# Kernel tuning notes

Measured on AMD Instinct MI355X. Metric: run time of the kernel, lower is better.

## Reference

```python
import jax, jax.numpy as jnp
import numpy as np
from jax import lax
from jax.scipy.special import logsumexp

B, S, H = 64, 512, 768
NUM_TAG, NUM_POS = 17, 45


def setup_inputs() -> dict:
    key = jax.random.key(0)
    ks = jax.random.split(key, 12)
    return {
        "hidden": jax.random.normal(ks[0], (B, S, H), dtype=jnp.float32),
        "mask": jnp.ones((B, S), dtype=jnp.int32),
        "target_tag": jax.random.randint(ks[1], (B, S), 0, NUM_TAG).astype(jnp.int64),
        "target_pos": jax.random.randint(ks[2], (B, S), 0, NUM_POS).astype(jnp.int64),
        "W_tag": jax.random.normal(ks[3], (H, NUM_TAG), dtype=jnp.float32) * 0.02,
        "b_tag": jnp.zeros((NUM_TAG,), dtype=jnp.float32),
        "W_pos": jax.random.normal(ks[4], (H, NUM_POS), dtype=jnp.float32) * 0.02,
        "b_pos": jnp.zeros((NUM_POS,), dtype=jnp.float32),
        "start_tag": jax.random.normal(ks[5], (NUM_TAG,), dtype=jnp.float32) * 0.1,
        "trans_tag": jax.random.normal(ks[6], (NUM_TAG, NUM_TAG), dtype=jnp.float32) * 0.1,
        "end_tag": jax.random.normal(ks[7], (NUM_TAG,), dtype=jnp.float32) * 0.1,
        "start_pos": jax.random.normal(ks[8], (NUM_POS,), dtype=jnp.float32) * 0.1,
        "trans_pos": jax.random.normal(ks[9], (NUM_POS, NUM_POS), dtype=jnp.float32) * 0.1,
        "end_pos": jax.random.normal(ks[10], (NUM_POS,), dtype=jnp.float32) * 0.1,
    }


def crf_nll(emissions, tags, mask, start, trans, end):
    """torchcrf negative log-likelihood, reduction='mean'. emissions:[B,S,T]."""
    e = jnp.swapaxes(emissions, 0, 1)            # [S,B,T]
    tg = jnp.swapaxes(tags, 0, 1)                # [S,B]
    m = jnp.swapaxes(mask, 0, 1).astype(emissions.dtype)  # [S,B]
    # --- numerator: score of the target path ---
    first = start[tg[0]] + jnp.take_along_axis(e[0], tg[0][:, None], 1)[:, 0]

    def num_step(carry, x):
        prev_tag, score = carry
        et, tt, mt = x
        s = trans[prev_tag, tt] + jnp.take_along_axis(et, tt[:, None], 1)[:, 0]
        score = score + s * mt
        prev_tag = jnp.where(mt > 0, tt, prev_tag)
        return (prev_tag, score), None

    (last_tag, num), _ = lax.scan(num_step, (tg[0], first), (e[1:], tg[1:], m[1:]))
    num = num + end[last_tag]
    # --- denominator: forward algorithm (log-sum-exp scan) ---
    score0 = start[None, :] + e[0]               # [B,T]

    def den_step(score, x):
        et, mt = x
        nxt = logsumexp(score[:, :, None] + trans[None, :, :] + et[:, None, :], axis=1)
        return jnp.where(mt[:, None] > 0, nxt, score), None

    den, _ = lax.scan(den_step, score0, (e[1:], m[1:]))
    den = logsumexp(den + end[None, :], axis=1)
    return -jnp.mean(num - den)


def crf_decode(emissions, mask, start, trans, end):
    """Viterbi decode; returns best tag paths [B,S] (int32)."""
    T = emissions.shape[-1]
    e = jnp.swapaxes(emissions, 0, 1)            # [S,B,T]
    m = jnp.swapaxes(mask, 0, 1)                 # [S,B]
    score0 = start[None, :] + e[0]

    def fwd_step(score, x):
        et, mt = x
        cand = score[:, :, None] + trans[None, :, :]     # [B,T,T]
        idx = jnp.argmax(cand, axis=1).astype(jnp.int32)  # [B,T] best prev tag
        nxt = jnp.max(cand, axis=1) + et
        keep = (mt > 0)[:, None]
        score = jnp.where(keep, nxt, score)
        idx = jnp.where(keep, idx, jnp.arange(T, dtype=jnp.int32)[None, :])
        return score, idx

    score, hist = lax.scan(fwd_step, score0, (e[1:], m[1:]))  # hist:[S-1,B,T]
    score = score + end[None, :]
    last = jnp.argmax(score, axis=1).astype(jnp.int32)        # [B]

    def back_step(tag, idx):
        prev = jnp.take_along_axis(idx, tag[:, None], 1)[:, 0]
        return prev, tag

    tag0, path = lax.scan(back_step, last, hist, reverse=True)  # path:[S-1,B]
    full = jnp.concatenate([tag0[None, :], path], axis=0)       # [S,B]
    return jnp.swapaxes(full, 0, 1)


def reference(hidden, mask, target_tag, target_pos,
              W_tag, b_tag, W_pos, b_pos,
              start_tag, trans_tag, end_tag,
              start_pos, trans_pos, end_pos):
    # dropout is identity in eval mode
    tag = jnp.einsum('bsh,ht->bst', hidden, W_tag) + b_tag   # [B,S,T]
    pos = jnp.einsum('bsh,hp->bsp', hidden, W_pos) + b_pos   # [B,S,P]
    loss_tag = crf_nll(jax.nn.log_softmax(tag, axis=2), target_tag, mask,
                       start_tag, trans_tag, end_tag)
    loss_pos = crf_nll(jax.nn.log_softmax(pos, axis=2), target_pos, mask,
                       start_pos, trans_pos, end_pos)
    pred_tag = crf_decode(tag, mask, start_tag, trans_tag, end_tag)
    pred_pos = crf_decode(pos, mask, start_pos, trans_pos, end_pos)
    return pred_tag, pred_pos, loss_tag, loss_pos
```

## Files before the change

### kernel.cpp

```cpp
#include <hip/hip_runtime.h>
#include <cmath>
#include <cstdint>
#include <cstddef>

#define NT 17
#define NP 45
#define CH 8

__device__ __forceinline__ float rlane(float v, int k) {
    return __int_as_float(__builtin_amdgcn_readlane(__float_as_int(v), k));
}

__global__ __launch_bounds__(256) void gemm_logits(
    const float* __restrict__ hidden, const float* __restrict__ Wt,
    const float* __restrict__ bt, const float* __restrict__ Wp,
    const float* __restrict__ bp, float* __restrict__ tagL,
    float* __restrict__ posL)
{
    __shared__ float As[32 * 68];
    __shared__ float Bs[32 * 64];
    const int tid = threadIdx.x;
    const int rg = tid >> 4;
    const int cg = tid & 15;
    const int row0 = blockIdx.x * 64;

    float acc[4][4];
#pragma unroll
    for (int a = 0; a < 4; ++a)
#pragma unroll
        for (int b = 0; b < 4; ++b) acc[a][b] = 0.f;

    for (int kc = 0; kc < 768; kc += 32) {
        __syncthreads();
#pragma unroll
        for (int it = 0; it < 2; ++it) {
            int idx = tid + it * 256;
            int r = idx >> 3, q = idx & 7;
            float4 h = *(const float4*)(hidden + (size_t)(row0 + r) * 768 + kc + q * 4);
            As[(q * 4 + 0) * 68 + r] = h.x;
            As[(q * 4 + 1) * 68 + r] = h.y;
            As[(q * 4 + 2) * 68 + r] = h.z;
            As[(q * 4 + 3) * 68 + r] = h.w;
        }
#pragma unroll
        for (int it = 0; it < 8; ++it) {
            int idx = tid + it * 256;
            int k = idx >> 6, c = idx & 63;
            float v = 0.f;
            if (c < NT) v = Wt[(kc + k) * NT + c];
            else if (c < NT + NP) v = Wp[(kc + k) * NP + (c - NT)];
            Bs[idx] = v;
        }
        __syncthreads();
#pragma unroll
        for (int kk = 0; kk < 32; ++kk) {
            float4 a4 = *(const float4*)(As + kk * 68 + rg * 4);
            float4 b4 = *(const float4*)(Bs + kk * 64 + cg * 4);
            float av[4] = {a4.x, a4.y, a4.z, a4.w};
            float bv[4] = {b4.x, b4.y, b4.z, b4.w};
#pragma unroll
            for (int jr = 0; jr < 4; ++jr)
#pragma unroll
                for (int jc = 0; jc < 4; ++jc)
                    acc[jr][jc] = fmaf(av[jr], bv[jc], acc[jr][jc]);
        }
    }
#pragma unroll
    for (int jr = 0; jr < 4; ++jr) {
        size_t r = (size_t)row0 + rg * 4 + jr;
#pragma unroll
        for (int jc = 0; jc < 4; ++jc) {
            int c = cg * 4 + jc;
            if (c < NT) tagL[r * NT + c] = acc[jr][jc] + bt[c];
            else if (c < NT + NP) posL[r * NP + (c - NT)] = acc[jr][jc] + bp[c - NT];
        }
    }
}

template <int T, int PAD>
__device__ void nll_scan(int b,
    const float* __restrict__ logits, const int* __restrict__ mask,
    const int* __restrict__ targ, const float* __restrict__ start,
    const float* __restrict__ trans, const float* __restrict__ endv,
    float* __restrict__ den, float* __restrict__ num)
{
    const int lane = threadIdx.x;
    const int jj = (lane < T) ? lane : (T - 1);
    float Ecol[PAD];
#pragma unroll
    for (int i = 0; i < PAD; ++i) Ecol[i] = (i < T) ? __expf(trans[i * T + jj]) : 0.f;
    const float esjj = __expf(start[jj]);
    const float* eptr = logits + (size_t)b * 512 * T + jj;
    const int* mptr = mask + b * 512;

    float eb[CH], en[CH], fb[CH];
    int mb, mn = 0;
#pragma unroll
    for (int k = 0; k < CH; ++k) { eb[k] = eptr[k * T]; en[k] = 0.f; }
    mb = mptr[lane & (CH - 1)];

    float a = 0.f;
    int excorr = 0;
    for (int c = 0; c < 64; ++c) {
        unsigned long long kb = __ballot(mb > 0);
        if (c < 63) {
            const float* ep2 = eptr + (c + 1) * CH * T;
#pragma unroll
            for (int k = 0; k < CH; ++k) en[k] = ep2[k * T];
            mn = mptr[(c + 1) * CH + (lane & (CH - 1))];
        }
#pragma unroll
        for (int k = 0; k < CH; ++k) fb[k] = __expf(eb[k]);
#pragma unroll
        for (int s = 0; s < CH; ++s) {
            float d0 = 0.f, d1 = 0.f, d2 = 0.f, d3 = 0.f;
#pragma unroll
            for (int q = 0; q < PAD / 4; ++q) {
                d0 = fmaf(rlane(a, 4 * q + 0), Ecol[4 * q + 0], d0);
                d1 = fmaf(rlane(a, 4 * q + 1), Ecol[4 * q + 1], d1);
                d2 = fmaf(rlane(a, 4 * q + 2), Ecol[4 * q + 2], d2);
                d3 = fmaf(rlane(a, 4 * q + 3), Ecol[4 * q + 3], d3);
            }
            float cand = ((d0 + d1) + (d2 + d3)) * fb[s];
            bool keep = (kb >> s) & 1ULL;
            bool first = (c == 0) && (s == 0);
            a = first ? (esjj * fb[0]) : (keep ? cand : a);
        }
        float m = a;
#pragma unroll
        for (int o = 32; o; o >>= 1) m = fmaxf(m, __shfl_xor(m, o));
        int ex;
        (void)frexpf(m, &ex);
        a *= ldexpf(1.0f, -ex);
        excorr += ex;
#pragma unroll
        for (int k = 0; k < CH; ++k) eb[k] = en[k];
        mb = mn;
    }
    float term = (lane < T) ? a * __expf(endv[lane]) : 0.f;
#pragma unroll
    for (int o = 32; o; o >>= 1) term += __shfl_xor(term, o);
    if (lane == 0) den[b] = __logf(term) + (float)excorr * 0.69314718056f;

    float part = 0.f; int Lc = 0;
    for (int t = lane; t < 512; t += 64) {
        int mt = mask[b * 512 + t];
        Lc += (mt > 0);
        if (t >= 1 && mt > 0) {
            int tg = targ[b * 512 + t];
            int pg = targ[b * 512 + t - 1];
            part += trans[pg * T + tg] + logits[((size_t)b * 512 + t) * T + tg];
        }
    }
#pragma unroll
    for (int o = 32; o; o >>= 1) { part += __shfl_xor(part, o); Lc += __shfl_xor(Lc, o); }
    if (lane == 0) {
        int t0g = targ[b * 512];
        num[b] = start[t0g] + logits[(size_t)b * 512 * T + t0g]
               + part + endv[targ[b * 512 + Lc - 1]];
    }
}

template <int T, int PAD>
__device__ void vit_fwd(int b,
    const float* __restrict__ logits, const int* __restrict__ mask,
    const float* __restrict__ start, const float* __restrict__ trans,
    float* __restrict__ score)
{
    const int lane = threadIdx.x;
    const int jj = (lane < T) ? lane : (T - 1);
    float Tcol[PAD];
#pragma unroll
    for (int i = 0; i < PAD; ++i) Tcol[i] = (i < T) ? trans[i * T + jj] : -1e30f;
    const float sjj = start[jj];
    const float* eptr = logits + (size_t)b * 512 * T + jj;
    const int* mptr = mask + b * 512;
    float* sptr = score + (size_t)b * 512 * T + lane;

    float eb[CH], en[CH];
    int mb, mn = 0;
#pragma unroll
    for (int k = 0; k < CH; ++k) { eb[k] = eptr[k * T]; en[k] = 0.f; }
    mb = mptr[lane & (CH - 1)];

    float sc = 0.f;
    for (int c = 0; c < 64; ++c) {
        unsigned long long kb = __ballot(mb > 0);
        if (c < 63) {
            const float* ep2 = eptr + (c + 1) * CH * T;
#pragma unroll
            for (int k = 0; k < CH; ++k) en[k] = ep2[k * T];
            mn = mptr[(c + 1) * CH + (lane & (CH - 1))];
        }
#pragma unroll
        for (int s = 0; s < CH; ++s) {
            float m = -1e30f;
#pragma unroll
            for (int q = 0; q < PAD / 4; ++q) {
                float ca = rlane(sc, 4 * q + 0) + Tcol[4 * q + 0];
                float cb = rlane(sc, 4 * q + 1) + Tcol[4 * q + 1];
                float cc = rlane(sc, 4 * q + 2) + Tcol[4 * q + 2];
                float cd = rlane(sc, 4 * q + 3) + Tcol[4 * q + 3];
                m = fmaxf(m, fmaxf(ca, cb));
                m = fmaxf(m, fmaxf(cc, cd));
            }
            float nxt = m + eb[s];
            bool keep = (kb >> s) & 1ULL;
            bool first = (c == 0) && (s == 0);
            sc = first ? (sjj + eb[0]) : (keep ? nxt : sc);
            if (lane < T) sptr[(size_t)(c * CH + s) * T] = sc;
        }
#pragma unroll
        for (int k = 0; k < CH; ++k) eb[k] = en[k];
        mb = mn;
    }
}

__global__ __launch_bounds__(64, 1) void scan_kernel(
    const float* tagL, const float* posL, const int* mask,
    const int* tgT, const int* tgP,
    const float* startT, const float* transT, const float* endT,
    const float* startP, const float* transP, const float* endP,
    float* scoreT, float* scoreP,
    float* denT, float* denP, float* numT, float* numP)
{
    int bid = blockIdx.x;
    if (bid < 64)
        vit_fwd<NP, 48>(bid, posL, mask, startP, transP, scoreP);
    else if (bid < 128)
        nll_scan<NP, 48>(bid - 64, posL, mask, tgP, startP, transP, endP, denP, numP);
    else if (bid < 192)
        vit_fwd<NT, 20>(bid - 128, tagL, mask, startT, transT, scoreT);
    else
        nll_scan<NT, 20>(bid - 192, tagL, mask, tgT, startT, transT, endT, denT, numT);
}

template <int T>
__device__ void hist_block(int b, int tc,
    const float* __restrict__ score, const int* __restrict__ mask,
    const float* __restrict__ trans, unsigned char* __restrict__ hist)
{
    const int wave = threadIdx.x >> 6;
    const int lane = threadIdx.x & 63;
    const int jj = (lane < T) ? lane : (T - 1);
    float Tcol[T];
#pragma unroll
    for (int i = 0; i < T; ++i) Tcol[i] = trans[i * T + jj];
    for (int q = 0; q < 16; ++q) {
        int t = tc * 64 + wave * 16 + q;
        if (t < 1) continue;
        int mt = mask[b * 512 + t];
        int hv;
        if (mt > 0) {
            float sv = score[((size_t)b * 512 + t - 1) * T + jj];
            float mx = -1e30f; int am = 0;
#pragma unroll
            for (int i = 0; i < T; ++i) {
                float cand = rlane(sv, i) + Tcol[i];
                bool g = cand > mx;
                mx = g ? cand : mx;
                am = g ? i : am;
            }
            hv = am;
        } else {
            hv = jj;
        }
        if (lane < T)
            hist[((size_t)b * 512 + (t - 1)) * T + lane] = (unsigned char)hv;
    }
}

__global__ __launch_bounds__(256) void hist_kernel(
    const float* scoreT, const float* scoreP, const int* mask,
    const float* transT, const float* transP,
    unsigned char* histT, unsigned char* histP)
{
    int blk = blockIdx.x;
    if (blk < 512) hist_block<NP>(blk >> 3, blk & 7, scoreP, mask, transP, histP);
    else { blk -= 512; hist_block<NT>(blk >> 3, blk & 7, scoreT, mask, transT, histT); }
}

template <int T>
__device__ void backtrace(int b, const float* __restrict__ score,
    const unsigned char* __restrict__ hist, const float* __restrict__ endv,
    float* __restrict__ outp, unsigned char* sh)
{
    unsigned char* h  = sh;
    unsigned char* g2 = sh + 512 * T;
    unsigned char* g4 = sh + 1024 * T;
    unsigned char* g8 = sh + 1024 * T + 128 * T;
    unsigned char* pr = sh + 1024 * T + 192 * T;
    const int lane = threadIdx.x;

    {
        const int4* src = (const int4*)(hist + (size_t)b * 512 * T);
        int4* dst = (int4*)h;
        int n16 = (512 * T) / 16;
        for (int i = lane; i < n16; i += 64) dst[i] = src[i];
    }
    __syncthreads();
    for (int idx = lane; idx < 510 * T; idx += 64) {
        int r = idx / T, i = idx - r * T;
        g2[idx] = h[r * T + h[(r + 1) * T + i]];
    }
    __syncthreads();
    for (int idx = lane; idx < 127 * T; idx += 64) {
        int a4 = idx / T, i = idx - a4 * T;
        int r = 3 + 4 * a4;
        g4[idx] = g2[r * T + g2[(r + 2) * T + i]];
    }
    __syncthreads();
    for (int idx = lane; idx < 63 * T; idx += 64) {
        int a = idx / T, i = idx - a * T;
        int r = 503 - 8 * a;
        int a4lo = (r - 3) >> 2, a4hi = (r + 1) >> 2;
        g8[idx] = g4[a4lo * T + g4[a4hi * T + i]];
    }
    float v = (lane < T) ? (score[((size_t)b * 512 + 511) * T + lane] + endv[lane]) : -1e30f;
    float mx = v;
#pragma unroll
    for (int o = 32; o; o >>= 1) mx = fmaxf(mx, __shfl_xor(mx, o));
    unsigned long long bal = __ballot(v == mx);
    int cur = __ffsll(bal) - 1;
    __syncthreads();
    int myCur = 0;
    for (int a = 0; a < 64; ++a) {
        if (lane == a) myCur = cur;
        if (a < 63) cur = g8[a * T + cur];
    }
    {
        int ta = 511 - 8 * lane;
        int j = myCur;
        pr[ta] = (unsigned char)j;
        int rlo = (lane == 63) ? 0 : (ta - 7);
        for (int r = ta - 1; r >= rlo; --r) {
            j = h[r * T + j];
            pr[r] = (unsigned char)j;
        }
    }
    __syncthreads();
    for (int k = lane; k < 512; k += 64)
        outp[(size_t)b * 512 + k] = (float)pr[k];
}

__global__ __launch_bounds__(64, 1) void backtrace_kernel(
    const float* scoreT, const float* scoreP,
    const unsigned char* histT, const unsigned char* histP,
    const float* endT, const float* endP, float* out)
{
    __shared__ __align__(16) unsigned char sh[1216 * NP + 576];
    int blk = blockIdx.x;
    if (blk < 64) backtrace<NP>(blk, scoreP, histP, endP, out + 32768, sh);
    else backtrace<NT>(blk - 64, scoreT, histT, endT, out, sh);
}

__global__ __launch_bounds__(64) void finalize_kernel(
    const float* numT, const float* denT, const float* numP, const float* denP,
    float* out)
{
    int lane = threadIdx.x;
    float dT = numT[lane] - denT[lane];
    float dP = numP[lane] - denP[lane];
#pragma unroll
    for (int o = 32; o; o >>= 1) { dT += __shfl_xor(dT, o); dP += __shfl_xor(dP, o); }
    if (lane == 0) {
        out[65536] = -dT / 64.f;
        out[65537] = -dP / 64.f;
    }
}

extern "C" void kernel_launch(void* const* d_in, const int* in_sizes, int n_in,
                              void* d_out, int out_size, void* d_ws, size_t ws_size,
                              hipStream_t stream)
{
    const float* hidden = (const float*)d_in[0];
    const int*   mask   = (const int*)d_in[1];
    const int*   tgT    = (const int*)d_in[2];
    const int*   tgP    = (const int*)d_in[3];
    const float* Wt     = (const float*)d_in[4];
    const float* bt     = (const float*)d_in[5];
    const float* Wp     = (const float*)d_in[6];
    const float* bp     = (const float*)d_in[7];
    const float* startT = (const float*)d_in[8];
    const float* transT = (const float*)d_in[9];
    const float* endT   = (const float*)d_in[10];
    const float* startP = (const float*)d_in[11];
    const float* transP = (const float*)d_in[12];
    const float* endP   = (const float*)d_in[13];

    float* ws     = (float*)d_ws;
    float* tagL   = ws;
    float* posL   = tagL + 557056;
    float* scoreT = posL + 1474560;
    float* scoreP = scoreT + 557056;
    float* denT   = scoreP + 1474560;
    float* denP   = denT + 64;
    float* numT   = denP + 64;
    float* numP   = numT + 64;
    unsigned char* histT = (unsigned char*)(numP + 64);
    unsigned char* histP = histT + (size_t)64 * 512 * NT;
    float* out = (float*)d_out;

    gemm_logits<<<512, 256, 0, stream>>>(hidden, Wt, bt, Wp, bp, tagL, posL);
    scan_kernel<<<256, 64, 0, stream>>>(tagL, posL, mask, tgT, tgP,
        startT, transT, endT, startP, transP, endP,
        scoreT, scoreP, denT, denP, numT, numP);
    hist_kernel<<<1024, 256, 0, stream>>>(scoreT, scoreP, mask, transT, transP,
        histT, histP);
    backtrace_kernel<<<128, 64, 0, stream>>>(scoreT, scoreP, histT, histP,
        endT, endP, out);
    finalize_kernel<<<1, 64, 0, stream>>>(numT, denT, numP, denP, out);
}
```

Measured before the change: 498.9 us.

## Rewrite logits GEMM as LDS-free wave-per-8-rows kernel with broadcast hidden loads

Replaces the shared-memory tiled GEMM with a design where each lane owns one output column (62 total) and each wave computes 8 rows. Hidden rows are read as uniform 8-float vector loads, the same for every lane, and weights are prefetched one k-chunk ahead in registers. The grid doubles to 1024 blocks of 32 rows each. The aim is to drop the LDS staging and the barriers on a memory-bound skinny GEMM, at the cost of strided uncoalesced weight loads and two idle lanes per wave.

```diff
diff --git a/kernel.cpp b/kernel.cpp
--- a/kernel.cpp
+++ b/kernel.cpp
@@ -6,6 +6,8 @@
 #define NT 17
 #define NP 45
 #define CH 8
+
+typedef float f32x8 __attribute__((ext_vector_type(8)));
 
 __device__ __forceinline__ float rlane(float v, int k) {
     return __int_as_float(__builtin_amdgcn_readlane(__float_as_int(v), k));
@@ -17,62 +19,57 @@
     const float* __restrict__ bp, float* __restrict__ tagL,
     float* __restrict__ posL)
 {
-    __shared__ float As[32 * 68];
-    __shared__ float Bs[32 * 64];
-    const int tid = threadIdx.x;
-    const int rg = tid >> 4;
-    const int cg = tid & 15;
-    const int row0 = blockIdx.x * 64;
-
-    float acc[4][4];
-#pragma unroll
-    for (int a = 0; a < 4; ++a)
-#pragma unroll
-        for (int b = 0; b < 4; ++b) acc[a][b] = 0.f;
-
-    for (int kc = 0; kc < 768; kc += 32) {
-        __syncthreads();
-#pragma unroll
-        for (int it = 0; it < 2; ++it) {
-            int idx = tid + it * 256;
-            int r = idx >> 3, q = idx & 7;
-            float4 h = *(const float4*)(hidden + (size_t)(row0 + r) * 768 + kc + q * 4);
-            As[(q * 4 + 0) * 68 + r] = h.x;
-            As[(q * 4 + 1) * 68 + r] = h.y;
-            As[(q * 4 + 2) * 68 + r] = h.z;
-            As[(q * 4 + 3) * 68 + r] = h.w;
-        }
-#pragma unroll
-        for (int it = 0; it < 8; ++it) {
-            int idx = tid + it * 256;
-            int k = idx >> 6, c = idx & 63;
-            float v = 0.f;
-            if (c < NT) v = Wt[(kc + k) * NT + c];
-            else if (c < NT + NP) v = Wp[(kc + k) * NP + (c - NT)];
-            Bs[idx] = v;
-        }
-        __syncthreads();
-#pragma unroll
-        for (int kk = 0; kk < 32; ++kk) {
-            float4 a4 = *(const float4*)(As + kk * 68 + rg * 4);
-            float4 b4 = *(const float4*)(Bs + kk * 64 + cg * 4);
-            float av[4] = {a4.x, a4.y, a4.z, a4.w};
-            float bv[4] = {b4.x, b4.y, b4.z, b4.w};
-#pragma unroll
-            for (int jr = 0; jr < 4; ++jr)
-#pragma unroll
-                for (int jc = 0; jc < 4; ++jc)
-                    acc[jr][jc] = fmaf(av[jr], bv[jc], acc[jr][jc]);
-        }
-    }
-#pragma unroll
-    for (int jr = 0; jr < 4; ++jr) {
-        size_t r = (size_t)row0 + rg * 4 + jr;
-#pragma unroll
-        for (int jc = 0; jc < 4; ++jc) {
-            int c = cg * 4 + jc;
-            if (c < NT) tagL[r * NT + c] = acc[jr][jc] + bt[c];
-            else if (c < NT + NP) posL[r * NP + (c - NT)] = acc[jr][jc] + bp[c - NT];
+    const int lane = threadIdx.x & 63;
+    const int wid  = __builtin_amdgcn_readfirstlane(threadIdx.x >> 6);
+    const int c = (lane < 62) ? lane : 61;
+    const bool isTag = (c < NT);
+    const float* wbase = isTag ? (Wt + c) : (Wp + (c - NT));
+    const int wstride = isTag ? NT : NP;
+    const float bias = isTag ? bt[c] : bp[c - NT];
+
+    const int row0 = blockIdx.x * 32 + wid * 8;
+    const float* h0 = hidden + (size_t)row0 * 768;
+
+    float acc[8];
+#pragma unroll
+    for (int r = 0; r < 8; ++r) acc[r] = 0.f;
+
+    float wv[8], wn[8];
+#pragma unroll
+    for (int j = 0; j < 8; ++j) wv[j] = wbase[(size_t)j * wstride];
+
+    for (int kc = 0; kc < 768; kc += 8) {
+        if (kc + 8 < 768) {
+#pragma unroll
+            for (int j = 0; j < 8; ++j)
+                wn[j] = wbase[(size_t)(kc + 8 + j) * wstride];
+        }
+        f32x8 hv[8];
+#pragma unroll
+        for (int r = 0; r < 8; ++r)
+            hv[r] = *(const f32x8*)(h0 + (size_t)r * 768 + kc);
+#pragma unroll
+        for (int r = 0; r < 8; ++r) {
+            acc[r] = fmaf(hv[r][0], wv[0], acc[r]);
+            acc[r] = fmaf(hv[r][1], wv[1], acc[r]);
+            acc[r] = fmaf(hv[r][2], wv[2], acc[r]);
+            acc[r] = fmaf(hv[r][3], wv[3], acc[r]);
+            acc[r] = fmaf(hv[r][4], wv[4], acc[r]);
+            acc[r] = fmaf(hv[r][5], wv[5], acc[r]);
+            acc[r] = fmaf(hv[r][6], wv[6], acc[r]);
+            acc[r] = fmaf(hv[r][7], wv[7], acc[r]);
+        }
+#pragma unroll
+        for (int j = 0; j < 8; ++j) wv[j] = wn[j];
+    }
+
+    if (lane < 62) {
+#pragma unroll
+        for (int r = 0; r < 8; ++r) {
+            float v = acc[r] + bias;
+            size_t row = (size_t)row0 + r;
+            if (isTag) tagL[row * NT + c] = v;
+            else       posL[row * NP + (c - NT)] = v;
         }
     }
 }
@@ -401,7 +398,7 @@
     unsigned char* histP = histT + (size_t)64 * 512 * NT;
     float* out = (float*)d_out;
 
-    gemm_logits<<<512, 256, 0, stream>>>(hidden, Wt, bt, Wp, bp, tagL, posL);
+    gemm_logits<<<1024, 256, 0, stream>>>(hidden, Wt, bt, Wp, bp, tagL, posL);
     scan_kernel<<<256, 64, 0, stream>>>(tagL, posL, mask, tgT, tgP,
         startT, transT, endT, startP, transP, endP,
         scoreT, scoreP, denT, denP, numT, numP);
```

Measured after the change: 538.8 us. 1.08x slower.

## Use direct global-to-LDS loads with swizzled A tile and prepacked weights in GEMM

Applied to the files above, without the earlier changes.

Adds a pre-pass that packs the tag and POS weight matrices into one zero-padded 768x64 buffer, so the GEMM can load B tiles with plain 16-byte loads. Both A and B tiles now go straight from global memory into LDS through the async global_load_lds builtin, and the A tile is stored row-major with an XOR swizzle instead of being transposed through registers. The inner loop is restructured into 4-wide k chunks. Separately, the scan's per-chunk max reduction now reads only the first T lanes with readlane instead of doing a full 64-lane shuffle. The packed weights live in the scoreT workspace region, which scan_kernel overwrites later, and this adds one extra kernel launch.

```diff
diff --git a/kernel.cpp b/kernel.cpp
--- a/kernel.cpp
+++ b/kernel.cpp
@@ -11,17 +11,36 @@
     return __int_as_float(__builtin_amdgcn_readlane(__float_as_int(v), k));
 }
 
+__device__ __forceinline__ void gload16(const float* g, float* l) {
+    __builtin_amdgcn_global_load_lds(
+        (const __attribute__((address_space(1))) void*)g,
+        (__attribute__((address_space(3))) void*)l, 16, 0, 0);
+}
+
+__global__ __launch_bounds__(256) void pack_w(
+    const float* __restrict__ Wt, const float* __restrict__ Wp,
+    float* __restrict__ Wpk)
+{
+    int i = blockIdx.x * 256 + threadIdx.x;
+    if (i >= 768 * 64) return;
+    int k = i >> 6, c = i & 63;
+    float v = 0.f;
+    if (c < NT) v = Wt[k * NT + c];
+    else if (c < NT + NP) v = Wp[k * NP + (c - NT)];
+    Wpk[i] = v;
+}
+
 __global__ __launch_bounds__(256) void gemm_logits(
-    const float* __restrict__ hidden, const float* __restrict__ Wt,
-    const float* __restrict__ bt, const float* __restrict__ Wp,
-    const float* __restrict__ bp, float* __restrict__ tagL,
-    float* __restrict__ posL)
-{
-    __shared__ float As[32 * 68];
-    __shared__ float Bs[32 * 64];
+    const float* __restrict__ hidden, const float* __restrict__ Wpk,
+    const float* __restrict__ bt, const float* __restrict__ bp,
+    float* __restrict__ tagL, float* __restrict__ posL)
+{
+    __shared__ __align__(16) float As[64 * 32];
+    __shared__ __align__(16) float Bs[32 * 64];
     const int tid = threadIdx.x;
     const int rg = tid >> 4;
     const int cg = tid & 15;
+    const int srg = rg & 7;
     const int row0 = blockIdx.x * 64;
 
     float acc[4][4];
@@ -30,40 +49,51 @@
 #pragma unroll
         for (int b = 0; b < 4; ++b) acc[a][b] = 0.f;
 
+    const int arow = tid >> 3;
+    const int aq   = tid & 7;
+    const int bk   = tid >> 4;
+    const int bc4  = tid & 15;
+
+#pragma unroll 1
     for (int kc = 0; kc < 768; kc += 32) {
+        {
+            int r0 = arow;
+            int s0 = (r0 >> 2) & 7;
+            gload16(hidden + (size_t)(row0 + r0) * 768 + kc + ((aq ^ s0) << 2),
+                    As + r0 * 32 + aq * 4);
+            int r1 = 32 + arow;
+            int s1 = (r1 >> 2) & 7;
+            gload16(hidden + (size_t)(row0 + r1) * 768 + kc + ((aq ^ s1) << 2),
+                    As + r1 * 32 + aq * 4);
+            gload16(Wpk + (size_t)(kc + bk) * 64 + bc4 * 4,
+                    Bs + bk * 64 + bc4 * 4);
+            gload16(Wpk + (size_t)(kc + 16 + bk) * 64 + bc4 * 4,
+                    Bs + (16 + bk) * 64 + bc4 * 4);
+        }
         __syncthreads();
 #pragma unroll
-        for (int it = 0; it < 2; ++it) {
-            int idx = tid + it * 256;
-            int r = idx >> 3, q = idx & 7;
-            float4 h = *(const float4*)(hidden + (size_t)(row0 + r) * 768 + kc + q * 4);
-            As[(q * 4 + 0) * 68 + r] = h.x;
-            As[(q * 4 + 1) * 68 + r] = h.y;
-            As[(q * 4 + 2) * 68 + r] = h.z;
-            As[(q * 4 + 3) * 68 + r] = h.w;
-        }
-#pragma unroll
-        for (int it = 0; it < 8; ++it) {
-            int idx = tid + it * 256;
-            int k = idx >> 6, c = idx & 63;
-            float v = 0.f;
-            if (c < NT) v = Wt[(kc + k) * NT + c];
-            else if (c < NT + NP) v = Wp[(kc + k) * NP + (c - NT)];
-            Bs[idx] = v;
+        for (int k4 = 0; k4 < 8; ++k4) {
+            const int qb = ((k4 ^ srg) << 2);
+            float a_[4][4], b_[4][4];
+#pragma unroll
+            for (int jr = 0; jr < 4; ++jr) {
+                float4 t = *(const float4*)(As + (rg * 4 + jr) * 32 + qb);
+                a_[jr][0] = t.x; a_[jr][1] = t.y; a_[jr][2] = t.z; a_[jr][3] = t.w;
+            }
+#pragma unroll
+            for (int kk = 0; kk < 4; ++kk) {
+                float4 t = *(const float4*)(Bs + (k4 * 4 + kk) * 64 + cg * 4);
+                b_[kk][0] = t.x; b_[kk][1] = t.y; b_[kk][2] = t.z; b_[kk][3] = t.w;
+            }
+#pragma unroll
+            for (int kk = 0; kk < 4; ++kk)
+#pragma unroll
+                for (int jr = 0; jr < 4; ++jr)
+#pragma unroll
+                    for (int jc = 0; jc < 4; ++jc)
+                        acc[jr][jc] = fmaf(a_[jr][kk], b_[kk][jc], acc[jr][jc]);
         }
         __syncthreads();
-#pragma unroll
-        for (int kk = 0; kk < 32; ++kk) {
-            float4 a4 = *(const float4*)(As + kk * 68 + rg * 4);
-            float4 b4 = *(const float4*)(Bs + kk * 64 + cg * 4);
-            float av[4] = {a4.x, a4.y, a4.z, a4.w};
-            float bv[4] = {b4.x, b4.y, b4.z, b4.w};
-#pragma unroll
-            for (int jr = 0; jr < 4; ++jr)
-#pragma unroll
-                for (int jc = 0; jc < 4; ++jc)
-                    acc[jr][jc] = fmaf(av[jr], bv[jc], acc[jr][jc]);
-        }
     }
 #pragma unroll
     for (int jr = 0; jr < 4; ++jr) {
@@ -126,9 +156,16 @@
             bool first = (c == 0) && (s == 0);
             a = first ? (esjj * fb[0]) : (keep ? cand : a);
         }
-        float m = a;
-#pragma unroll
-        for (int o = 32; o; o >>= 1) m = fmaxf(m, __shfl_xor(m, o));
+        float mv0 = rlane(a, 0), mv1 = rlane(a, 1);
+        float mv2 = rlane(a, 2), mv3 = rlane(a, 3);
+#pragma unroll
+        for (int i = 4; i < T; i += 4) {
+            mv0 = fmaxf(mv0, rlane(a, i + 0));
+            mv1 = fmaxf(mv1, rlane(a, i + 1));
+            mv2 = fmaxf(mv2, rlane(a, i + 2));
+            mv3 = fmaxf(mv3, rlane(a, i + 3));
+        }
+        float m = fmaxf(fmaxf(mv0, mv1), fmaxf(mv2, mv3));
         int ex;
         (void)frexpf(m, &ex);
         a *= ldexpf(1.0f, -ex);
@@ -401,7 +438,10 @@
     unsigned char* histP = histT + (size_t)64 * 512 * NT;
     float* out = (float*)d_out;
 
-    gemm_logits<<<512, 256, 0, stream>>>(hidden, Wt, bt, Wp, bp, tagL, posL);
+    float* Wpk = scoreT;
+
+    pack_w<<<192, 256, 0, stream>>>(Wt, Wp, Wpk);
+    gemm_logits<<<512, 256, 0, stream>>>(hidden, Wpk, bt, bp, tagL, posL);
     scan_kernel<<<256, 64, 0, stream>>>(tagL, posL, mask, tgT, tgP,
         startT, transT, endT, startP, transP, endP,
         scoreT, scoreP, denT, denP, numT, numP);
```

After: 412.4 us. -17.3%, faster.
